# Kernel tuning notes

Hardware: AMD Instinct MI355X
Metric: run time of the kernel (lower is better)

## Reference

```python
import jax, jax.numpy as jnp
import numpy as np

B, T, S = 4, 16, 4096
H, KV, D, DIM = 32, 8, 128, 4096
BASE = 10000.0
START = 2048
SCALE = 1.0 / np.sqrt(D)


def _rope(t, cos, sin):
    # t: [B, T, nh, D]; ggml 'normal' rope rotates adjacent pairs (x[2i], x[2i+1])
    b, tt, nh, d = t.shape
    t2 = t.reshape(b, tt, nh, d // 2, 2)
    x0, x1 = t2[..., 0], t2[..., 1]
    c = cos[None, :, None, :]  # [1, T, 1, D/2]
    s = sin[None, :, None, :]
    r = jnp.stack([x0 * c - x1 * s, x0 * s + x1 * c], axis=-1)
    return r.reshape(b, tt, nh, d)


def setup_inputs() -> dict:
    key = jax.random.key(0)
    ks = jax.random.split(key, 8)
    x = jax.random.normal(ks[0], (B, T, DIM), dtype=jnp.float32)
    k_cache = jax.random.normal(ks[1], (B, S, KV, D), dtype=jnp.float32)
    v_cache = jax.random.normal(ks[2], (B, S, KV, D), dtype=jnp.float32)
    wq = jax.random.normal(ks[3], (H * D, DIM), dtype=jnp.float32) * 0.02
    wk = jax.random.normal(ks[4], (KV * D, DIM), dtype=jnp.float32) * 0.02
    wv = jax.random.normal(ks[5], (KV * D, DIM), dtype=jnp.float32) * 0.02
    wo = jax.random.normal(ks[6], (DIM, H * D), dtype=jnp.float32) * 0.02
    input_pos = jnp.arange(T, dtype=jnp.int32) + START  # contiguous decode chunk
    inv_freq = BASE ** (-jnp.arange(0, D, 2, dtype=jnp.float32) / D)  # [D/2]
    ang = input_pos.astype(jnp.float32)[:, None] * inv_freq[None, :]  # [T, D/2]
    freqs_cos = jnp.cos(ang)
    freqs_sin = jnp.sin(ang)
    # causal mask: kv position <= query absolute position, [T, S] bool
    attn_mask = jnp.arange(S, dtype=jnp.int32)[None, :] <= input_pos[:, None]
    return {"x": x, "freqs_cos": freqs_cos, "freqs_sin": freqs_sin,
            "input_pos": input_pos, "attn_mask": attn_mask,
            "k_cache": k_cache, "v_cache": v_cache,
            "wq": wq, "wk": wk, "wv": wv, "wo": wo}


def reference(x, freqs_cos, freqs_sin, input_pos, attn_mask, k_cache, v_cache, wq, wk, wv, wo):
    b, t, _ = x.shape
    q = (x @ wq.T).reshape(b, t, H, D)
    k = (x @ wk.T).reshape(b, t, KV, D)
    v = (x @ wv.T).reshape(b, t, KV, D)
    q = _rope(q, freqs_cos, freqs_sin)
    k = _rope(k, freqs_cos, freqs_sin)
    # KV-cache scatter (index_copy_ along dim 1)
    kc = k_cache.at[:, input_pos].set(k)  # [B, S, KV, D]
    vc = v_cache.at[:, input_pos].set(v)
    g = H // KV
    qh = q.transpose(0, 2, 1, 3).reshape(b, KV, g, t, D)  # [B, KV, g, T, D]
    kf = kc.transpose(0, 2, 1, 3)  # [B, KV, S, D]
    vf = vc.transpose(0, 2, 1, 3)
    scores = jnp.einsum('bkgtd,bksd->bkgts', qh, kf) * SCALE
    scores = jnp.where(attn_mask[None, None, None], scores, jnp.finfo(scores.dtype).min)
    probs = jax.nn.softmax(scores, axis=-1)
    y = jnp.einsum('bkgts,bksd->bkgtd', probs, vf)  # [B, KV, g, T, D]
    y = y.reshape(b, H, t, D).transpose(0, 2, 1, 3).reshape(b, t, H * D)
    return y @ wo.T
```

## Files before the change

### kernel.cpp

```cpp
#include <hip/hip_runtime.h>


#define SCALE_F 0.08838834764831845f

typedef __attribute__((ext_vector_type(8))) short bf16x8;
typedef __attribute__((ext_vector_type(4))) float f32x4;

__device__ __forceinline__ unsigned short f2b(float f) {
    union { float f; unsigned u; } v; v.f = f;
    unsigned r = v.u + 0x7FFFu + ((v.u >> 16) & 1u);
    return (unsigned short)(r >> 16);
}

__device__ __forceinline__ bf16x8 pack8(float4 a, float4 b) {
    bf16x8 r;
    r[0] = (short)f2b(a.x); r[1] = (short)f2b(a.y); r[2] = (short)f2b(a.z); r[3] = (short)f2b(a.w);
    r[4] = (short)f2b(b.x); r[5] = (short)f2b(b.y); r[6] = (short)f2b(b.z); r[7] = (short)f2b(b.w);
    return r;
}

__global__ __launch_bounds__(256) void qkv_gemm_kernel(
    const float* __restrict__ x,
    const float* __restrict__ wq, const float* __restrict__ wk, const float* __restrict__ wvp,
    float* __restrict__ part)
{
    __shared__ unsigned short a_lds[64][258];
    const int tid = threadIdx.x, lane = tid & 63, wid = tid >> 6;
    const int k_base = blockIdx.y * 256;

    {
        const int sr = tid >> 2, sq = tid & 3;
        const float* xp = x + (size_t)sr * 4096 + k_base;
        #pragma unroll
        for (int j = 0; j < 8; ++j) {
            int col = 32 * j + 8 * sq;
            float4 p0 = *(const float4*)(xp + col);
            float4 p1 = *(const float4*)(xp + col + 4);
            *(bf16x8*)&a_lds[sr][col] = pack8(p0, p1);
        }
    }
    __syncthreads();

    const int n0 = blockIdx.x * 128 + wid * 32;
    const float* wptr; int nn;
    if (n0 < 4096)      { wptr = wq;  nn = n0; }
    else if (n0 < 5120) { wptr = wk;  nn = n0 - 4096; }
    else                { wptr = wvp; nn = n0 - 5120; }

    const int l15 = lane & 15, lh = lane >> 4;
    const float* w0 = wptr + (size_t)(nn + l15) * 4096 + k_base + 8 * lh;
    const float* w1 = w0 + 16 * 4096;

    float4 buf0[4], buf1[4];
#define ISSUE0(S) do { buf0[0]=*(const float4*)(w0+(S)*32); buf0[1]=*(const float4*)(w0+(S)*32+4); \
                       buf0[2]=*(const float4*)(w1+(S)*32); buf0[3]=*(const float4*)(w1+(S)*32+4); } while(0)
#define ISSUE1(S) do { buf1[0]=*(const float4*)(w0+(S)*32); buf1[1]=*(const float4*)(w0+(S)*32+4); \
                       buf1[2]=*(const float4*)(w1+(S)*32); buf1[3]=*(const float4*)(w1+(S)*32+4); } while(0)

    f32x4 acc[4][2];
    #pragma unroll
    for (int m = 0; m < 4; ++m) { acc[m][0] = (f32x4){0,0,0,0}; acc[m][1] = (f32x4){0,0,0,0}; }

    ISSUE0(0); ISSUE1(1);
    #pragma unroll
    for (int s = 0; s < 8; ++s) {
        bf16x8 b0, b1;
        if ((s & 1) == 0) { b0 = pack8(buf0[0], buf0[1]); b1 = pack8(buf0[2], buf0[3]); if (s < 6) ISSUE0(s + 2); }
        else              { b0 = pack8(buf1[0], buf1[1]); b1 = pack8(buf1[2], buf1[3]); if (s < 6) ISSUE1(s + 2); }
        #pragma unroll
        for (int m = 0; m < 4; ++m) {
            bf16x8 a = *(bf16x8*)&a_lds[16 * m + l15][s * 32 + 8 * lh];
            acc[m][0] = __builtin_amdgcn_mfma_f32_16x16x32_bf16(a, b0, acc[m][0], 0, 0, 0);
            acc[m][1] = __builtin_amdgcn_mfma_f32_16x16x32_bf16(a, b1, acc[m][1], 0, 0, 0);
        }
    }
#undef ISSUE0
#undef ISSUE1

    float* pp = part + (size_t)blockIdx.y * 64 * 6144;
    #pragma unroll
    for (int m = 0; m < 4; ++m)
        #pragma unroll
        for (int nh = 0; nh < 2; ++nh)
            #pragma unroll
            for (int r = 0; r < 4; ++r)
                pp[(16 * m + 4 * lh + r) * 6144 + n0 + nh * 16 + l15] = acc[m][nh][r];
}

__global__ __launch_bounds__(256) void qkv_reduce_kernel(
    const float* __restrict__ part,
    const float* __restrict__ fcos, const float* __restrict__ fsin,
    unsigned short* __restrict__ q_out, unsigned short* __restrict__ k_new,
    unsigned short* __restrict__ v_new)
{
    const int gid = blockIdx.x * 256 + threadIdx.x;
    const int m = gid / 1536;
    const int n = (gid % 1536) * 4;
    float4 s = {0.f,0.f,0.f,0.f};
    #pragma unroll
    for (int sp = 0; sp < 16; ++sp) {
        float4 v = *(const float4*)(part + (size_t)(sp * 64 + m) * 6144 + n);
        s.x += v.x; s.y += v.y; s.z += v.z; s.w += v.w;
    }
    const int t = m & 15, b = m >> 4;
    ushort4 o;
    if (n < 5120) {
        int d = n & 127;
        float c0 = fcos[t * 64 + (d >> 1)],     s0 = fsin[t * 64 + (d >> 1)];
        float c1 = fcos[t * 64 + (d >> 1) + 1], s1 = fsin[t * 64 + (d >> 1) + 1];
        o.x = f2b(s.x * c0 - s.y * s0);
        o.y = f2b(s.x * s0 + s.y * c0);
        o.z = f2b(s.z * c1 - s.w * s1);
        o.w = f2b(s.z * s1 + s.w * c1);
    } else {
        o.x = f2b(s.x); o.y = f2b(s.y); o.z = f2b(s.z); o.w = f2b(s.w);
    }
    if (n < 4096) {
        int h = n >> 7, d = n & 127;
        int row = (b * 8 + (h >> 2)) * 64 + (h & 3) * 16 + t;
        *(ushort4*)(q_out + row * 128 + d) = o;
    } else if (n < 5120) {
        int idx = n - 4096, kvh = idx >> 7, d = idx & 127;
        *(ushort4*)(k_new + ((b * 8 + kvh) * 16 + t) * 128 + d) = o;
    } else {
        int idx = n - 5120, kvh = idx >> 7, d = idx & 127;
        *(ushort4*)(v_new + ((b * 8 + kvh) * 16 + t) * 128 + d) = o;
    }
}

__global__ __launch_bounds__(256) void attn_kernel(
    const float* __restrict__ k_cache, const float* __restrict__ v_cache,
    const unsigned short* __restrict__ q_glob,
    const unsigned short* __restrict__ k_new, const unsigned short* __restrict__ v_new,
    float* __restrict__ y_part, float* __restrict__ ml)
{
    __shared__ unsigned short smem[32256];
    unsigned short* kv_lds = smem;
    unsigned short* p_lds  = smem + 21504;

    const int bk = blockIdx.x >> 4;
    const int c  = blockIdx.x & 15;
    const int b = bk >> 3, kvh = bk & 7;
    const int tid = threadIdx.x, lane = tid & 63, wid = tid >> 6;
    const int s0 = c * 128;
    const bool last = (c == 15);

    bf16x8 aq[4];
    {
        const unsigned short* qp = q_glob + (bk * 64 + 16 * wid + (lane & 15)) * 128 + 8 * (lane >> 4);
        #pragma unroll
        for (int kk = 0; kk < 4; ++kk) aq[kk] = *(const bf16x8*)(qp + kk * 32);
    }

    const int rr = tid >> 5, ln4 = (tid & 31) * 4;
    {
        const float* kb = k_cache + ((size_t)(b * 4096 + s0) * 8 + kvh) * 128;
        #pragma unroll 4
        for (int it = 0; it < 16; ++it) {
            int srow = it * 8 + rr;
            float4 kf = *(const float4*)(kb + (size_t)srow * 1024 + ln4);
            ushort4 k4; k4.x = f2b(kf.x); k4.y = f2b(kf.y); k4.z = f2b(kf.z); k4.w = f2b(kf.w);
            *(ushort4*)&kv_lds[srow * 136 + ln4] = k4;
        }
        if (last) {
            int row = tid >> 4, c8 = (tid & 15) * 8;
            *(bf16x8*)&kv_lds[(128 + row) * 136 + c8] =
                *(const bf16x8*)(k_new + (bk * 16 + row) * 128 + c8);
        }
    }
    __syncthreads();

    f32x4 sc[9];
    f32x4 zero4 = {0.f,0.f,0.f,0.f};
    #pragma unroll
    for (int st = 0; st < 9; ++st) sc[st] = zero4;
    #pragma unroll
    for (int kk = 0; kk < 4; ++kk) {
        #pragma unroll
        for (int st = 0; st < 9; ++st) {
            if (st == 8 && !last) continue;
            bf16x8 bf = *(bf16x8*)&kv_lds[(st * 16 + (lane & 15)) * 136 + kk * 32 + 8 * (lane >> 4)];
            sc[st] = __builtin_amdgcn_mfma_f32_16x16x32_bf16(aq[kk], bf, sc[st], 0, 0, 0);
        }
    }

    float mrow[4], lrow[4];
    #pragma unroll
    for (int r = 0; r < 4; ++r) {
        int trow = 4 * (lane >> 4) + r;
        float mx = -3.0e38f;
        #pragma unroll
        for (int st = 0; st < 9; ++st) {
            if (st == 8 && !last) continue;
            float s = sc[st][r] * SCALE_F;
            if (st == 8 && (lane & 15) > trow) s = -3.0e38f;
            sc[st][r] = s;
            mx = fmaxf(mx, s);
        }
        mx = fmaxf(mx, __shfl_xor(mx, 1));
        mx = fmaxf(mx, __shfl_xor(mx, 2));
        mx = fmaxf(mx, __shfl_xor(mx, 4));
        mx = fmaxf(mx, __shfl_xor(mx, 8));
        float sum = 0.f;
        #pragma unroll
        for (int st = 0; st < 9; ++st) {
            if (st == 8 && !last) continue;
            float p = __expf(sc[st][r] - mx);
            sc[st][r] = p;
            sum += p;
        }
        sum += __shfl_xor(sum, 1);
        sum += __shfl_xor(sum, 2);
        sum += __shfl_xor(sum, 4);
        sum += __shfl_xor(sum, 8);
        mrow[r] = mx; lrow[r] = sum;
    }

    #pragma unroll
    for (int st = 0; st < 9; ++st) {
        if (st == 8 && !last) continue;
        #pragma unroll
        for (int r = 0; r < 4; ++r)
            p_lds[(16 * wid + 4 * (lane >> 4) + r) * 168 + st * 16 + (lane & 15)] = f2b(sc[st][r]);
    }
    if ((lane & 15) == 0) {
        #pragma unroll
        for (int r = 0; r < 4; ++r) {
            int row = 16 * wid + 4 * (lane >> 4) + r;
            ml[(bk * 16 + c) * 128 + row * 2 + 0] = mrow[r];
            ml[(bk * 16 + c) * 128 + row * 2 + 1] = lrow[r];
        }
    }
    __syncthreads();

    {
        const float* vb = v_cache + ((size_t)(b * 4096 + s0) * 8 + kvh) * 128;
        #pragma unroll 4
        for (int it = 0; it < 16; ++it) {
            int srow = it * 8 + rr;
            float4 vf = *(const float4*)(vb + (size_t)srow * 1024 + ln4);
            kv_lds[(ln4 + 0) * 168 + srow] = f2b(vf.x);
            kv_lds[(ln4 + 1) * 168 + srow] = f2b(vf.y);
            kv_lds[(ln4 + 2) * 168 + srow] = f2b(vf.z);
            kv_lds[(ln4 + 3) * 168 + srow] = f2b(vf.w);
        }
        if (last) {
            int row = tid >> 4, c8 = (tid & 15) * 8;
            bf16x8 vv = *(const bf16x8*)(v_new + (bk * 16 + row) * 128 + c8);
            #pragma unroll
            for (int u = 0; u < 8; ++u)
                kv_lds[(c8 + u) * 168 + 128 + row] = (unsigned short)vv[u];
            int pr = tid >> 2, pc = (tid & 3) * 4;
            #pragma unroll
            for (int u = 0; u < 4; ++u) p_lds[pr * 168 + 144 + pc + u] = 0;
            int vr = tid >> 1, vc = (tid & 1) * 8;
            #pragma unroll
            for (int u = 0; u < 8; ++u) kv_lds[vr * 168 + 144 + vc + u] = 0;
        }
    }
    __syncthreads();

    f32x4 o_[8];
    #pragma unroll
    for (int nt = 0; nt < 8; ++nt) o_[nt] = zero4;
    #pragma unroll
    for (int ks = 0; ks < 5; ++ks) {
        if (ks == 4 && !last) continue;
        bf16x8 a = *(bf16x8*)&p_lds[(16 * wid + (lane & 15)) * 168 + ks * 32 + 8 * (lane >> 4)];
        #pragma unroll
        for (int nt = 0; nt < 8; ++nt) {
            bf16x8 bf = *(bf16x8*)&kv_lds[(nt * 16 + (lane & 15)) * 168 + ks * 32 + 8 * (lane >> 4)];
            o_[nt] = __builtin_amdgcn_mfma_f32_16x16x32_bf16(a, bf, o_[nt], 0, 0, 0);
        }
    }
    float* yp = y_part + (size_t)(bk * 16 + c) * 8192;
    #pragma unroll
    for (int nt = 0; nt < 8; ++nt) {
        #pragma unroll
        for (int r = 0; r < 4; ++r)
            yp[(16 * wid + 4 * (lane >> 4) + r) * 128 + nt * 16 + (lane & 15)] = o_[nt][r];
    }
}

__global__ __launch_bounds__(256) void combine_kernel(
    const float* __restrict__ y_part, const float* __restrict__ ml,
    unsigned short* __restrict__ y_attn)
{
    const int bid = blockIdx.x;
    const int bk = bid >> 3, rg = bid & 7;
    const int b = bk >> 3, kvh = bk & 7;
    const int tid = threadIdx.x;
    const int d = tid & 127, r2 = tid >> 7;
    for (int rr = 0; rr < 8; rr += 2) {
        int row = rg * 8 + rr + r2;
        float mv[16], lv[16], M = -3.0e38f;
        #pragma unroll
        for (int cc = 0; cc < 16; ++cc) {
            mv[cc] = ml[(bk * 16 + cc) * 128 + row * 2 + 0];
            lv[cc] = ml[(bk * 16 + cc) * 128 + row * 2 + 1];
            M = fmaxf(M, mv[cc]);
        }
        float den = 0.f, acc = 0.f;
        #pragma unroll
        for (int cc = 0; cc < 16; ++cc) {
            float co = __expf(mv[cc] - M);
            den += co * lv[cc];
            acc += co * y_part[((size_t)(bk * 16 + cc) * 64 + row) * 128 + d];
        }
        float y = acc / den;
        int gi = row >> 4, t = row & 15;
        y_attn[(b * 16 + t) * 4096 + (kvh * 4 + gi) * 128 + d] = f2b(y);
    }
}

__global__ __launch_bounds__(256) void proj_gemm_kernel(
    const unsigned short* __restrict__ y_attn, const float* __restrict__ wo,
    float* __restrict__ part)
{
    __shared__ unsigned short a_lds[64][258];
    const int tid = threadIdx.x, lane = tid & 63, wid = tid >> 6;
    const int k_base = blockIdx.y * 256;

    {
        const int sr = tid >> 2, sq = tid & 3;
        const unsigned short* ap = y_attn + (size_t)sr * 4096 + k_base;
        #pragma unroll
        for (int j = 0; j < 8; ++j) {
            int col = 32 * j + 8 * sq;
            *(bf16x8*)&a_lds[sr][col] = *(const bf16x8*)(ap + col);
        }
    }
    __syncthreads();

    const int n0 = blockIdx.x * 128 + wid * 32;
    const int l15 = lane & 15, lh = lane >> 4;
    const float* w0 = wo + (size_t)(n0 + l15) * 4096 + k_base + 8 * lh;
    const float* w1 = w0 + 16 * 4096;

    float4 buf0[4], buf1[4];
#define ISSUE0(S) do { buf0[0]=*(const float4*)(w0+(S)*32); buf0[1]=*(const float4*)(w0+(S)*32+4); \
                       buf0[2]=*(const float4*)(w1+(S)*32); buf0[3]=*(const float4*)(w1+(S)*32+4); } while(0)
#define ISSUE1(S) do { buf1[0]=*(const float4*)(w0+(S)*32); buf1[1]=*(const float4*)(w0+(S)*32+4); \
                       buf1[2]=*(const float4*)(w1+(S)*32); buf1[3]=*(const float4*)(w1+(S)*32+4); } while(0)

    f32x4 acc[4][2];
    #pragma unroll
    for (int m = 0; m < 4; ++m) { acc[m][0] = (f32x4){0,0,0,0}; acc[m][1] = (f32x4){0,0,0,0}; }

    ISSUE0(0); ISSUE1(1);
    #pragma unroll
    for (int s = 0; s < 8; ++s) {
        bf16x8 b0, b1;
        if ((s & 1) == 0) { b0 = pack8(buf0[0], buf0[1]); b1 = pack8(buf0[2], buf0[3]); if (s < 6) ISSUE0(s + 2); }
        else              { b0 = pack8(buf1[0], buf1[1]); b1 = pack8(buf1[2], buf1[3]); if (s < 6) ISSUE1(s + 2); }
        #pragma unroll
        for (int m = 0; m < 4; ++m) {
            bf16x8 a = *(bf16x8*)&a_lds[16 * m + l15][s * 32 + 8 * lh];
            acc[m][0] = __builtin_amdgcn_mfma_f32_16x16x32_bf16(a, b0, acc[m][0], 0, 0, 0);
            acc[m][1] = __builtin_amdgcn_mfma_f32_16x16x32_bf16(a, b1, acc[m][1], 0, 0, 0);
        }
    }
#undef ISSUE0
#undef ISSUE1

    float* pp = part + (size_t)blockIdx.y * 64 * 4096;
    #pragma unroll
    for (int m = 0; m < 4; ++m)
        #pragma unroll
        for (int nh = 0; nh < 2; ++nh)
            #pragma unroll
            for (int r = 0; r < 4; ++r)
                pp[(16 * m + 4 * lh + r) * 4096 + n0 + nh * 16 + l15] = acc[m][nh][r];
}

__global__ __launch_bounds__(256) void proj_reduce_kernel(
    const float* __restrict__ part, float* __restrict__ out)
{
    const int gid = blockIdx.x * 256 + threadIdx.x;
    const int m = gid >> 10;
    const int n = (gid & 1023) * 4;
    float4 s = {0.f,0.f,0.f,0.f};
    #pragma unroll
    for (int sp = 0; sp < 16; ++sp) {
        float4 v = *(const float4*)(part + (size_t)(sp * 64 + m) * 4096 + n);
        s.x += v.x; s.y += v.y; s.z += v.z; s.w += v.w;
    }
    *(float4*)(out + (size_t)m * 4096 + n) = s;
}

extern "C" void kernel_launch(void* const* d_in, const int* in_sizes, int n_in,
                              void* d_out, int out_size, void* d_ws, size_t ws_size,
                              hipStream_t stream)
{
    const float* x       = (const float*)d_in[0];
    const float* fcos    = (const float*)d_in[1];
    const float* fsin    = (const float*)d_in[2];
    const float* k_cache = (const float*)d_in[5];
    const float* v_cache = (const float*)d_in[6];
    const float* wq      = (const float*)d_in[7];
    const float* wk      = (const float*)d_in[8];
    const float* wv      = (const float*)d_in[9];
    const float* wo      = (const float*)d_in[10];

    char* p = (char*)d_ws;
    unsigned short* q_out  = (unsigned short*)p; p += 4 * 8 * 64 * 128 * 2;
    unsigned short* k_new  = (unsigned short*)p; p += 4 * 8 * 16 * 128 * 2;
    unsigned short* v_new  = (unsigned short*)p; p += 4 * 8 * 16 * 128 * 2;
    unsigned short* y_attn = (unsigned short*)p; p += 64 * 4096 * 2;
    float* mlbuf  = (float*)p; p += 32 * 16 * 64 * 2 * 4;
    float* y_part = (float*)p; p += (size_t)32 * 16 * 64 * 128 * 4;
    float* bigbuf = (float*)p;

    qkv_gemm_kernel<<<dim3(48, 16), 256, 0, stream>>>(x, wq, wk, wv, bigbuf);
    qkv_reduce_kernel<<<384, 256, 0, stream>>>(bigbuf, fcos, fsin, q_out, k_new, v_new);
    attn_kernel<<<512, 256, 0, stream>>>(k_cache, v_cache, q_out, k_new, v_new, y_part, mlbuf);
    combine_kernel<<<256, 256, 0, stream>>>(y_part, mlbuf, y_attn);
    proj_gemm_kernel<<<dim3(32, 16), 256, 0, stream>>>(y_attn, wo, bigbuf);
    proj_reduce_kernel<<<256, 256, 0, stream>>>(bigbuf, (float*)d_out);
}
```

Before: 80.70 us.

## Stream GEMM weights via global_load_lds with swizzled LDS and smaller N tiles

Both weight GEMMs are restructured. Each block now covers 32 output columns with four waves splitting the 64 rows, and the fp32 weight tiles are copied straight from global memory into XOR-swizzled LDS with global_load_lds, in two groups so the first can be consumed while the second is still arriving. The activation operand is read from registers instead of LDS, so x is converted to bf16 once in a new small pre-kernel. The intent is to raise memory-level parallelism and occupancy on the bandwidth-bound weight streaming, at the cost of an extra launch, four times as many blocks, and hand-written vmcnt waits that are fragile.

```diff
diff --git a/kernel.cpp b/kernel.cpp
--- a/kernel.cpp
+++ b/kernel.cpp
@@ -1,4 +1,5 @@
 #include <hip/hip_runtime.h>
+#include <hip/hip_bf16.h>
 
 
 #define SCALE_F 0.08838834764831845f
@@ -7,9 +8,8 @@
 typedef __attribute__((ext_vector_type(4))) float f32x4;
 
 __device__ __forceinline__ unsigned short f2b(float f) {
-    union { float f; unsigned u; } v; v.f = f;
-    unsigned r = v.u + 0x7FFFu + ((v.u >> 16) & 1u);
-    return (unsigned short)(r >> 16);
+    __hip_bfloat16 h = __float2bfloat16(f);
+    return *reinterpret_cast<unsigned short*>(&h);
 }
 
 __device__ __forceinline__ bf16x8 pack8(float4 a, float4 b) {
@@ -19,72 +19,85 @@
     return r;
 }
 
+__device__ __forceinline__ void gl_lds16(const void* g, void* l) {
+    __builtin_amdgcn_global_load_lds(
+        (const __attribute__((address_space(1))) void*)g,
+        (__attribute__((address_space(3))) void*)l, 16, 0, 0);
+}
+
+__global__ __launch_bounds__(256) void xcvt_kernel(
+    const float* __restrict__ x, unsigned short* __restrict__ xb)
+{
+    const int i = (blockIdx.x * 256 + threadIdx.x) * 4;
+    float4 v = *(const float4*)(x + i);
+    ushort4 o; o.x = f2b(v.x); o.y = f2b(v.y); o.z = f2b(v.z); o.w = f2b(v.w);
+    *(ushort4*)(xb + i) = o;
+}
+
 __global__ __launch_bounds__(256) void qkv_gemm_kernel(
-    const float* __restrict__ x,
+    const unsigned short* __restrict__ xb,
     const float* __restrict__ wq, const float* __restrict__ wk, const float* __restrict__ wvp,
     float* __restrict__ part)
 {
-    __shared__ unsigned short a_lds[64][258];
+    __shared__ float wlds[2][16][256];
     const int tid = threadIdx.x, lane = tid & 63, wid = tid >> 6;
-    const int k_base = blockIdx.y * 256;
-
-    {
-        const int sr = tid >> 2, sq = tid & 3;
-        const float* xp = x + (size_t)sr * 4096 + k_base;
-        #pragma unroll
-        for (int j = 0; j < 8; ++j) {
-            int col = 32 * j + 8 * sq;
-            float4 p0 = *(const float4*)(xp + col);
-            float4 p1 = *(const float4*)(xp + col + 4);
-            *(bf16x8*)&a_lds[sr][col] = pack8(p0, p1);
-        }
-    }
-    __syncthreads();
-
-    const int n0 = blockIdx.x * 128 + wid * 32;
+    const int l15 = lane & 15, lh = lane >> 4;
+    const int n0 = blockIdx.x * 32;
+    const int kbase = blockIdx.y * 256;
+
     const float* wptr; int nn;
     if (n0 < 4096)      { wptr = wq;  nn = n0; }
     else if (n0 < 5120) { wptr = wk;  nn = n0 - 4096; }
     else                { wptr = wvp; nn = n0 - 5120; }
 
-    const int l15 = lane & 15, lh = lane >> 4;
-    const float* w0 = wptr + (size_t)(nn + l15) * 4096 + k_base + 8 * lh;
-    const float* w1 = w0 + 16 * 4096;
-
-    float4 buf0[4], buf1[4];
-#define ISSUE0(S) do { buf0[0]=*(const float4*)(w0+(S)*32); buf0[1]=*(const float4*)(w0+(S)*32+4); \
-                       buf0[2]=*(const float4*)(w1+(S)*32); buf0[3]=*(const float4*)(w1+(S)*32+4); } while(0)
-#define ISSUE1(S) do { buf1[0]=*(const float4*)(w0+(S)*32); buf1[1]=*(const float4*)(w0+(S)*32+4); \
-                       buf1[2]=*(const float4*)(w1+(S)*32); buf1[3]=*(const float4*)(w1+(S)*32+4); } while(0)
-
-    f32x4 acc[4][2];
-    #pragma unroll
-    for (int m = 0; m < 4; ++m) { acc[m][0] = (f32x4){0,0,0,0}; acc[m][1] = (f32x4){0,0,0,0}; }
-
-    ISSUE0(0); ISSUE1(1);
-    #pragma unroll
-    for (int s = 0; s < 8; ++s) {
-        bf16x8 b0, b1;
-        if ((s & 1) == 0) { b0 = pack8(buf0[0], buf0[1]); b1 = pack8(buf0[2], buf0[3]); if (s < 6) ISSUE0(s + 2); }
-        else              { b0 = pack8(buf1[0], buf1[1]); b1 = pack8(buf1[2], buf1[3]); if (s < 6) ISSUE1(s + 2); }
-        #pragma unroll
-        for (int m = 0; m < 4; ++m) {
-            bf16x8 a = *(bf16x8*)&a_lds[16 * m + l15][s * 32 + 8 * lh];
-            acc[m][0] = __builtin_amdgcn_mfma_f32_16x16x32_bf16(a, b0, acc[m][0], 0, 0, 0);
-            acc[m][1] = __builtin_amdgcn_mfma_f32_16x16x32_bf16(a, b1, acc[m][1], 0, 0, 0);
-        }
-    }
-#undef ISSUE0
-#undef ISSUE1
-
-    float* pp = part + (size_t)blockIdx.y * 64 * 6144;
-    #pragma unroll
-    for (int m = 0; m < 4; ++m)
-        #pragma unroll
-        for (int nh = 0; nh < 2; ++nh)
-            #pragma unroll
-            for (int r = 0; r < 4; ++r)
-                pp[(16 * m + 4 * lh + r) * 6144 + n0 + nh * 16 + l15] = acc[m][nh][r];
+    bf16x8 aq[8];
+    {
+        const unsigned short* ap = xb + (size_t)(16 * wid + l15) * 4096 + kbase + 8 * lh;
+        #pragma unroll
+        for (int t = 0; t < 8; ++t) aq[t] = *(const bf16x8*)(ap + t * 32);
+    }
+    asm volatile("" ::: "memory");
+
+    #pragma unroll
+    for (int g = 0; g < 2; ++g) {
+        #pragma unroll
+        for (int i = 0; i < 4; ++i) {
+            const int r = wid * 4 + i;
+            const float* src = wptr + (size_t)(nn + g * 16 + r) * 4096 + kbase
+                             + ((lane ^ (r & 7)) * 4);
+            gl_lds16(src, &wlds[g][r][0]);
+        }
+        asm volatile("" ::: "memory");
+    }
+
+    f32x4 acc[2];
+    acc[0] = (f32x4){0.f,0.f,0.f,0.f};
+    acc[1] = (f32x4){0.f,0.f,0.f,0.f};
+
+    const int key = l15 & 7;
+    #pragma unroll
+    for (int g = 0; g < 2; ++g) {
+        if (g == 0) asm volatile("s_waitcnt vmcnt(4)" ::: "memory");
+        else        asm volatile("s_waitcnt vmcnt(0)" ::: "memory");
+        __builtin_amdgcn_s_barrier();
+        const float* wrow = &wlds[g][l15][0];
+        #pragma unroll
+        for (int t = 0; t < 8; ++t) {
+            const int c0 = (t * 8 + 2 * lh) ^ key;
+            const int c1 = (t * 8 + 2 * lh + 1) ^ key;
+            float4 w0 = *(const float4*)(wrow + c0 * 4);
+            float4 w1 = *(const float4*)(wrow + c1 * 4);
+            bf16x8 b = pack8(w0, w1);
+            acc[g] = __builtin_amdgcn_mfma_f32_16x16x32_bf16(aq[t], b, acc[g], 0, 0, 0);
+        }
+    }
+
+    float* pp = part + (size_t)blockIdx.y * 64 * 6144 + n0;
+    #pragma unroll
+    for (int g = 0; g < 2; ++g)
+        #pragma unroll
+        for (int r = 0; r < 4; ++r)
+            pp[(16 * wid + 4 * lh + r) * 6144 + g * 16 + l15] = acc[g][r];
 }
 
 __global__ __launch_bounds__(256) void qkv_reduce_kernel(
@@ -317,60 +330,60 @@
     const unsigned short* __restrict__ y_attn, const float* __restrict__ wo,
     float* __restrict__ part)
 {
-    __shared__ unsigned short a_lds[64][258];
+    __shared__ float wlds[2][16][256];
     const int tid = threadIdx.x, lane = tid & 63, wid = tid >> 6;
-    const int k_base = blockIdx.y * 256;
-
+    const int l15 = lane & 15, lh = lane >> 4;
+    const int n0 = blockIdx.x * 32;
+    const int kbase = blockIdx.y * 256;
+
+    bf16x8 aq[8];
     {
-        const int sr = tid >> 2, sq = tid & 3;
-        const unsigned short* ap = y_attn + (size_t)sr * 4096 + k_base;
-        #pragma unroll
-        for (int j = 0; j < 8; ++j) {
-            int col = 32 * j + 8 * sq;
-            *(bf16x8*)&a_lds[sr][col] = *(const bf16x8*)(ap + col);
-        }
-    }
-    __syncthreads();
-
-    const int n0 = blockIdx.x * 128 + wid * 32;
-    const int l15 = lane & 15, lh = lane >> 4;
-    const float* w0 = wo + (size_t)(n0 + l15) * 4096 + k_base + 8 * lh;
-    const float* w1 = w0 + 16 * 4096;
-
-    float4 buf0[4], buf1[4];
-#define ISSUE0(S) do { buf0[0]=*(const float4*)(w0+(S)*32); buf0[1]=*(const float4*)(w0+(S)*32+4); \
-                       buf0[2]=*(const float4*)(w1+(S)*32); buf0[3]=*(const float4*)(w1+(S)*32+4); } while(0)
-#define ISSUE1(S) do { buf1[0]=*(const float4*)(w0+(S)*32); buf1[1]=*(const float4*)(w0+(S)*32+4); \
-                       buf1[2]=*(const float4*)(w1+(S)*32); buf1[3]=*(const float4*)(w1+(S)*32+4); } while(0)
-
-    f32x4 acc[4][2];
-    #pragma unroll
-    for (int m = 0; m < 4; ++m) { acc[m][0] = (f32x4){0,0,0,0}; acc[m][1] = (f32x4){0,0,0,0}; }
-
-    ISSUE0(0); ISSUE1(1);
-    #pragma unroll
-    for (int s = 0; s < 8; ++s) {
-        bf16x8 b0, b1;
-        if ((s & 1) == 0) { b0 = pack8(buf0[0], buf0[1]); b1 = pack8(buf0[2], buf0[3]); if (s < 6) ISSUE0(s + 2); }
-        else              { b0 = pack8(buf1[0], buf1[1]); b1 = pack8(buf1[2], buf1[3]); if (s < 6) ISSUE1(s + 2); }
-        #pragma unroll
-        for (int m = 0; m < 4; ++m) {
-            bf16x8 a = *(bf16x8*)&a_lds[16 * m + l15][s * 32 + 8 * lh];
-            acc[m][0] = __builtin_amdgcn_mfma_f32_16x16x32_bf16(a, b0, acc[m][0], 0, 0, 0);
-            acc[m][1] = __builtin_amdgcn_mfma_f32_16x16x32_bf16(a, b1, acc[m][1], 0, 0, 0);
-        }
-    }
-#undef ISSUE0
-#undef ISSUE1
-
-    float* pp = part + (size_t)blockIdx.y * 64 * 4096;
-    #pragma unroll
-    for (int m = 0; m < 4; ++m)
-        #pragma unroll
-        for (int nh = 0; nh < 2; ++nh)
-            #pragma unroll
-            for (int r = 0; r < 4; ++r)
-                pp[(16 * m + 4 * lh + r) * 4096 + n0 + nh * 16 + l15] = acc[m][nh][r];
+        const unsigned short* ap = y_attn + (size_t)(16 * wid + l15) * 4096 + kbase + 8 * lh;
+        #pragma unroll
+        for (int t = 0; t < 8; ++t) aq[t] = *(const bf16x8*)(ap + t * 32);
+    }
+    asm volatile("" ::: "memory");
+
+    #pragma unroll
+    for (int g = 0; g < 2; ++g) {
+        #pragma unroll
+        for (int i = 0; i < 4; ++i) {
+            const int r = wid * 4 + i;
+            const float* src = wo + (size_t)(n0 + g * 16 + r) * 4096 + kbase
+                             + ((lane ^ (r & 7)) * 4);
+            gl_lds16(src, &wlds[g][r][0]);
+        }
+        asm volatile("" ::: "memory");
+    }
+
+    f32x4 acc[2];
+    acc[0] = (f32x4){0.f,0.f,0.f,0.f};
+    acc[1] = (f32x4){0.f,0.f,0.f,0.f};
+
+    const int key = l15 & 7;
+    #pragma unroll
+    for (int g = 0; g < 2; ++g) {
+        if (g == 0) asm volatile("s_waitcnt vmcnt(4)" ::: "memory");
+        else        asm volatile("s_waitcnt vmcnt(0)" ::: "memory");
+        __builtin_amdgcn_s_barrier();
+        const float* wrow = &wlds[g][l15][0];
+        #pragma unroll
+        for (int t = 0; t < 8; ++t) {
+            const int c0 = (t * 8 + 2 * lh) ^ key;
+            const int c1 = (t * 8 + 2 * lh + 1) ^ key;
+            float4 w0 = *(const float4*)(wrow + c0 * 4);
+            float4 w1 = *(const float4*)(wrow + c1 * 4);
+            bf16x8 b = pack8(w0, w1);
+            acc[g] = __builtin_amdgcn_mfma_f32_16x16x32_bf16(aq[t], b, acc[g], 0, 0, 0);
+        }
+    }
+
+    float* pp = part + (size_t)blockIdx.y * 64 * 4096 + n0;
+    #pragma unroll
+    for (int g = 0; g < 2; ++g)
+        #pragma unroll
+        for (int r = 0; r < 4; ++r)
+            pp[(16 * wid + 4 * lh + r) * 4096 + g * 16 + l15] = acc[g][r];
 }
 
 __global__ __launch_bounds__(256) void proj_reduce_kernel(
@@ -407,14 +420,16 @@
     unsigned short* k_new  = (unsigned short*)p; p += 4 * 8 * 16 * 128 * 2;
     unsigned short* v_new  = (unsigned short*)p; p += 4 * 8 * 16 * 128 * 2;
     unsigned short* y_attn = (unsigned short*)p; p += 64 * 4096 * 2;
+    unsigned short* x_bf16 = (unsigned short*)p; p += 64 * 4096 * 2;
     float* mlbuf  = (float*)p; p += 32 * 16 * 64 * 2 * 4;
     float* y_part = (float*)p; p += (size_t)32 * 16 * 64 * 128 * 4;
     float* bigbuf = (float*)p;
 
-    qkv_gemm_kernel<<<dim3(48, 16), 256, 0, stream>>>(x, wq, wk, wv, bigbuf);
+    xcvt_kernel<<<256, 256, 0, stream>>>(x, x_bf16);
+    qkv_gemm_kernel<<<dim3(192, 16), 256, 0, stream>>>(x_bf16, wq, wk, wv, bigbuf);
     qkv_reduce_kernel<<<384, 256, 0, stream>>>(bigbuf, fcos, fsin, q_out, k_new, v_new);
     attn_kernel<<<512, 256, 0, stream>>>(k_cache, v_cache, q_out, k_new, v_new, y_part, mlbuf);
     combine_kernel<<<256, 256, 0, stream>>>(y_part, mlbuf, y_attn);
-    proj_gemm_kernel<<<dim3(32, 16), 256, 0, stream>>>(y_attn, wo, bigbuf);
+    proj_gemm_kernel<<<dim3(128, 16), 256, 0, stream>>>(y_attn, wo, bigbuf);
     proj_reduce_kernel<<<256, 256, 0, stream>>>(bigbuf, (float*)d_out);
 }
```

After: 97.39 us. +20.7%, slower.
